# Performance work log

Hardware: AMD Instinct MI355X
Metric: run time of the kernel (lower is better)

Reference implementation:

```python
import jax, jax.numpy as jnp
import numpy as np

B_, C_, T_, F_ = 1, 64, 256, 128
D_CONV, D_STATE, DT_RANK = 4, 16, 4
D_INNER = 2 * C_
EPS = 1e-5


def setup_inputs():
    key = jax.random.key(0)
    ks = jax.random.split(key, 12)
    s = 0.05
    return {
        'x': jax.random.normal(ks[0], (B_, C_, T_, F_), jnp.float32),
        'norm_w': jnp.ones((4, C_), jnp.float32),
        'in_proj_w': jax.random.normal(ks[1], (4, 2 * D_INNER, C_), jnp.float32) * s,
        'conv_w': jax.random.normal(ks[2], (4, D_INNER, 1, D_CONV), jnp.float32) * 0.3,
        'conv_b': jnp.zeros((4, D_INNER), jnp.float32),
        'x_proj_w': jax.random.normal(ks[3], (4, DT_RANK + 2 * D_STATE, D_INNER), jnp.float32) * s,
        'dt_proj_w': jax.random.normal(ks[4], (4, D_INNER, DT_RANK), jnp.float32) * 0.1,
        'dt_proj_b': jnp.log(jnp.expm1(jax.random.uniform(ks[5], (4, D_INNER), jnp.float32, 1e-3, 0.1))),
        'A_log': jnp.log(jax.random.uniform(ks[6], (4, D_INNER, D_STATE), jnp.float32, 0.5, 16.0)),
        'Dp': jnp.ones((4, D_INNER), jnp.float32),
        'out_proj_w': jax.random.normal(ks[7], (4, C_, D_INNER), jnp.float32) * s,
        'tlin_w': jax.random.normal(ks[8], (2 * C_, C_), jnp.float32) * s,
        'tlin_b': jnp.zeros((C_,), jnp.float32),
        'flin_w': jax.random.normal(ks[9], (2 * C_, C_), jnp.float32) * s,
        'flin_b': jnp.zeros((C_,), jnp.float32),
    }


def _rmsnorm(x, w):
    return x * jax.lax.rsqrt(jnp.mean(x * x, axis=-1, keepdims=True) + EPS) * w


def _mamba(u, p):
    # u: (N, L, d_model) ; selective-scan Mamba mixer
    N, L, _ = u.shape
    xz = jnp.einsum('nld,ed->nle', u, p['in_proj_w'])  # (N,L,2*di)
    x, z = jnp.split(xz, 2, axis=-1)
    # causal depthwise conv over time
    xT = jnp.swapaxes(x, 1, 2)  # (N, di, L)
    xc = jax.lax.conv_general_dilated(xT, p['conv_w'], (1,), [(D_CONV - 1, 0)],
                                      feature_group_count=D_INNER)
    x = jnp.swapaxes(jax.nn.silu(xc + p['conv_b'][None, :, None]), 1, 2)  # (N,L,di)
    xdbl = jnp.einsum('nld,ed->nle', x, p['x_proj_w'])
    dt, Bm, Cm = jnp.split(xdbl, [DT_RANK, DT_RANK + D_STATE], axis=-1)
    dt = jax.nn.softplus(jnp.einsum('nlr,dr->nld', dt, p['dt_proj_w']) + p['dt_proj_b'])
    A = -jnp.exp(p['A_log'])  # (di, ds)

    def step(h, inp):
        dt_t, B_t, C_t, x_t = inp  # (N,di),(N,ds),(N,ds),(N,di)
        dA = jnp.exp(dt_t[:, :, None] * A)  # (N,di,ds)
        h = dA * h + dt_t[:, :, None] * B_t[:, None, :] * x_t[:, :, None]
        return h, jnp.einsum('nds,ns->nd', h, C_t)

    h0 = jnp.zeros((N, D_INNER, D_STATE), u.dtype)
    _, ys = jax.lax.scan(step, h0, (jnp.swapaxes(dt, 0, 1), jnp.swapaxes(Bm, 0, 1),
                                    jnp.swapaxes(Cm, 0, 1), jnp.swapaxes(x, 0, 1)))
    y = jnp.swapaxes(ys, 0, 1) + x * p['Dp']
    y = y * jax.nn.silu(z)
    return jnp.einsum('nld,od->nlo', y, p['out_proj_w'])


def _block(u, p):
    # mamba Block with residual: out = mixer(rmsnorm(u)) + u
    return _mamba(_rmsnorm(u, p['norm_w']), p) + u


def _bimamba(u, pf, pb):
    yf = _block(u, pf)
    yb = jnp.flip(_block(jnp.flip(u, 1), pb), 1)
    return jnp.concatenate([yf, yb], axis=-1)


def _pick(i, norm_w, in_proj_w, conv_w, conv_b, x_proj_w, dt_proj_w, dt_proj_b, A_log, Dp, out_proj_w):
    return dict(norm_w=norm_w[i], in_proj_w=in_proj_w[i], conv_w=conv_w[i], conv_b=conv_b[i],
                x_proj_w=x_proj_w[i], dt_proj_w=dt_proj_w[i], dt_proj_b=dt_proj_b[i],
                A_log=A_log[i], Dp=Dp[i], out_proj_w=out_proj_w[i])


def _tfmamba(x, norm_w, in_proj_w, conv_w, conv_b, x_proj_w, dt_proj_w, dt_proj_b,
             A_log, Dp, out_proj_w, tlin_w, tlin_b, flin_w, flin_b):
    b, c, t, f = x.shape
    P = [_pick(i, norm_w, in_proj_w, conv_w, conv_b, x_proj_w, dt_proj_w, dt_proj_b, A_log, Dp, out_proj_w)
         for i in range(4)]
    # time axis
    xt = jnp.reshape(jnp.transpose(x, (0, 3, 2, 1)), (b * f, t, c))
    xt_out = _bimamba(xt, P[0], P[1])  # (b*f, t, 2c)
    xt = xt + jnp.einsum('nti,io->nto', xt_out, tlin_w) + tlin_b
    # frequency axis
    xf = jnp.reshape(jnp.transpose(jnp.reshape(xt, (b, f, t, c)), (0, 2, 1, 3)), (b * t, f, c))
    xf_out = _bimamba(xf, P[2], P[3])  # (b*t, f, 2c)
    xf = xf + jnp.einsum('nfi,io->nfo', xf_out, flin_w) + flin_b
    return jnp.transpose(jnp.reshape(xf, (b, t, f, c)), (0, 3, 1, 2))


def reference(x, norm_w, in_proj_w, conv_w, conv_b, x_proj_w, dt_proj_w, dt_proj_b,
              A_log, Dp, out_proj_w, tlin_w, tlin_b, flin_w, flin_b):
    return _tfmamba(x, norm_w, in_proj_w, conv_w, conv_b, x_proj_w, dt_proj_w, dt_proj_b,
                    A_log, Dp, out_proj_w, tlin_w, tlin_b, flin_w, flin_b)
```

## Files before the change

kernel.cpp:

```cpp
#include <hip/hip_runtime.h>
#include <math.h>

#define C_DIM 64
#define T_DIM 256
#define F_DIM 128
#define DI    128
#define DS    16
#define CK    16

typedef __attribute__((ext_vector_type(8))) short bf16x8;
typedef __attribute__((ext_vector_type(4))) float f32x4;

__device__ __forceinline__ float silu_f(float v){ return v / (1.0f + __expf(-v)); }

__device__ __forceinline__ unsigned short f2bf(float f){
  union{float f; unsigned u;} v; v.f = f;
  unsigned r = v.u + 0x7FFFu + ((v.u >> 16) & 1u);
  return (unsigned short)(r >> 16);
}

__global__ __launch_bounds__(256) void k_prep(const float* __restrict__ ipw,
                                              const float* __restrict__ opw,
                                              unsigned short* __restrict__ wbuf){
  const int i = blockIdx.x*256 + threadIdx.x;
  if(i < 65536)       wbuf[i] = f2bf(ipw[i]);
  else if(i < 98304)  wbuf[i] = f2bf(opw[i - 65536]);
}

__global__ __launch_bounds__(256) void k_transpose_in(const float* __restrict__ x,
                                                      float* __restrict__ xt){
  __shared__ float tile[64][133];
  const int t = blockIdx.x;
  {
    const int fi = threadIdx.x & 127, cg = threadIdx.x >> 7;
    for(int c = cg*32; c < cg*32 + 32; ++c)
      tile[c][fi] = x[(size_t)c*32768 + (size_t)t*128 + fi];
  }
  __syncthreads();
  {
    const int ci = threadIdx.x & 63, fg = threadIdx.x >> 6;
    for(int f = fg*32; f < fg*32 + 32; ++f)
      xt[(size_t)f*16384 + (size_t)t*64 + ci] = tile[ci][f];
  }
}

__global__ __launch_bounds__(256, 2) void k_mamba(
    const float* __restrict__ src, int N, int L, long long sn, long long sl,
    int pbase,
    const float* __restrict__ norm_w,   const unsigned short* __restrict__ wbf,
    const float* __restrict__ conv_w,   const float* __restrict__ conv_b,
    const float* __restrict__ x_proj_w, const float* __restrict__ dt_proj_w,
    const float* __restrict__ dt_proj_b,const float* __restrict__ A_log,
    const float* __restrict__ Dp,       float* __restrict__ obuf)
{
  __shared__ __align__(16) unsigned short u_bf[CK][64];
  __shared__ float x_s[CK+3][132];
  __shared__ float z_s[CK][132];
  __shared__ float xc_s[CK][132];
  __shared__ float dt_s[CK][132];
  __shared__ float dtr_s[CK][4];
  __shared__ float B_s[CK][20];
  __shared__ float C_s[CK][20];
  __shared__ __align__(16) unsigned short y_bf[CK][128];
  __shared__ float y_out[CK][68];
  __shared__ float w_xp[36*132];
  __shared__ float w_cv[512];
  __shared__ float b_cv[128];
  __shared__ float w_dt[512];
  __shared__ float b_dt[128];
  __shared__ float dvec[128];
  __shared__ float nw[64];

  const int tid = threadIdx.x;
  const int bid = blockIdx.x;
  const int dir = (bid >= N) ? 1 : 0;
  const int n   = dir ? (bid - N) : bid;
  const int p   = pbase + dir;

  const int lane = tid & 63;
  const int wv   = tid >> 6;
  const int fr   = lane & 15;
  const int fk   = (lane >> 4) << 3;

  for(int i = tid; i < 36*128; i += 256){
    int o = i >> 7, k = i & 127;
    w_xp[o*132 + k] = x_proj_w[p*4608 + i];
  }
  for(int i = tid; i < 512; i += 256){ w_cv[i] = conv_w[p*512 + i]; w_dt[i] = dt_proj_w[p*512 + i]; }
  if(tid < 128){ b_cv[tid] = conv_b[p*128 + tid]; b_dt[tid] = dt_proj_b[p*128 + tid]; dvec[tid] = Dp[p*128 + tid]; }
  if(tid < 64) nw[tid] = norm_w[p*64 + tid];
  for(int i = tid; i < 3*128; i += 256){ x_s[i >> 7][i & 127] = 0.0f; }

  const unsigned short* WinB  = wbf + (size_t)p*16384;
  const unsigned short* WoutB = wbf + 65536 + (size_t)p*8192;
  bf16x8 aW[4][2];
  #pragma unroll
  for(int ot = 0; ot < 4; ++ot)
    #pragma unroll
    for(int kh = 0; kh < 2; ++kh)
      aW[ot][kh] = *(const bf16x8*)(WinB + (wv*64 + ot*16 + fr)*64 + kh*32 + fk);
  bf16x8 aO[4];
  #pragma unroll
  for(int kc = 0; kc < 4; ++kc)
    aO[kc] = *(const bf16x8*)(WoutB + (wv*16 + fr)*128 + kc*32 + fk);

  const int d_own = tid >> 1;
  const int sh    = (tid & 1) * 8;
  float A_r[8], h[8];
  #pragma unroll
  for(int i = 0; i < 8; ++i){
    A_r[i] = -__expf(A_log[p*2048 + d_own*16 + sh + i]) * 1.44269504f;
    h[i] = 0.0f;
  }
  __syncthreads();

  for(int c0 = 0; c0 < L; c0 += CK){
    if(c0 > 0){
      for(int i = tid; i < 3*128; i += 256){
        int r = i >> 7, ch = i & 127;
        x_s[r][ch] = x_s[CK + r][ch];
      }
    }
    {
      const int g = tid >> 4, j = tid & 15, c4 = j*4;
      const int l = c0 + g;
      const int lo = dir ? (L - 1 - l) : l;
      const float4 v = *(const float4*)(src + (size_t)n*sn + (size_t)lo*sl + c4);
      float ssq = v.x*v.x + v.y*v.y + v.z*v.z + v.w*v.w;
      ssq += __shfl_xor(ssq, 1); ssq += __shfl_xor(ssq, 2);
      ssq += __shfl_xor(ssq, 4); ssq += __shfl_xor(ssq, 8);
      const float sc = rsqrtf(ssq * (1.0f/64.0f) + 1e-5f);
      ushort4 pk;
      pk.x = f2bf(v.x * sc * nw[c4+0]);
      pk.y = f2bf(v.y * sc * nw[c4+1]);
      pk.z = f2bf(v.z * sc * nw[c4+2]);
      pk.w = f2bf(v.w * sc * nw[c4+3]);
      *(ushort4*)&u_bf[g][c4] = pk;
    }
    __syncthreads();

    {
      const bf16x8 b0 = *(const bf16x8*)&u_bf[fr][fk];
      const bf16x8 b1 = *(const bf16x8*)&u_bf[fr][32 + fk];
      #pragma unroll
      for(int ot = 0; ot < 4; ++ot){
        f32x4 acc = {0.f, 0.f, 0.f, 0.f};
        acc = __builtin_amdgcn_mfma_f32_16x16x32_bf16(aW[ot][0], b0, acc, 0, 0, 0);
        acc = __builtin_amdgcn_mfma_f32_16x16x32_bf16(aW[ot][1], b1, acc, 0, 0, 0);
        const int ob = wv*64 + ot*16 + ((lane >> 4) << 2);
        if(wv < 2){
          #pragma unroll
          for(int r = 0; r < 4; ++r) x_s[3 + fr][ob + r] = acc[r];
        } else {
          #pragma unroll
          for(int r = 0; r < 4; ++r) z_s[fr][ob + r - 128] = acc[r];
        }
      }
    }
    __syncthreads();

    {
      const int g = tid >> 4, j = tid & 15;
      #pragma unroll
      for(int i = 0; i < 8; ++i){
        const int ch = j + 16*i;
        float a = b_cv[ch];
        a += w_cv[ch*4+0] * x_s[g+0][ch];
        a += w_cv[ch*4+1] * x_s[g+1][ch];
        a += w_cv[ch*4+2] * x_s[g+2][ch];
        a += w_cv[ch*4+3] * x_s[g+3][ch];
        xc_s[g][ch] = silu_f(a);
      }
    }
    __syncthreads();

    {
      const int g = tid >> 4, j = tid & 15;
      #pragma unroll
      for(int rep = 0; rep < 3; ++rep){
        const int o36 = j + rep*16;
        if(o36 < 36){
          const float4* wr = (const float4*)&w_xp[o36*132];
          const float4* xr = (const float4*)&xc_s[g][0];
          float a = 0.0f;
          #pragma unroll
          for(int k4 = 0; k4 < 32; ++k4){
            const float4 w = wr[k4], xv = xr[k4];
            a += w.x*xv.x + w.y*xv.y + w.z*xv.z + w.w*xv.w;
          }
          if(o36 < 4)       dtr_s[g][o36] = a;
          else if(o36 < 20) B_s[g][o36 - 4] = a;
          else              C_s[g][o36 - 20] = a;
        }
      }
    }
    __syncthreads();

    {
      const int g = tid >> 4, j = tid & 15;
      const float r0 = dtr_s[g][0], r1 = dtr_s[g][1], r2 = dtr_s[g][2], r3 = dtr_s[g][3];
      #pragma unroll
      for(int i = 0; i < 8; ++i){
        const int d = j + 16*i;
        float a = b_dt[d] + w_dt[d*4+0]*r0 + w_dt[d*4+1]*r1 + w_dt[d*4+2]*r2 + w_dt[d*4+3]*r3;
        dt_s[g][d] = fmaxf(a, 0.0f) + log1pf(__expf(-fabsf(a)));
      }
    }
    __syncthreads();

    for(int l = 0; l < CK; ++l){
      const float dtv = dt_s[l][d_own];
      const float xv  = xc_s[l][d_own];
      const float4 b0 = *(const float4*)&B_s[l][sh];
      const float4 b1 = *(const float4*)&B_s[l][sh + 4];
      const float4 g0 = *(const float4*)&C_s[l][sh];
      const float4 g1 = *(const float4*)&C_s[l][sh + 4];
      const float bb[8] = {b0.x,b0.y,b0.z,b0.w,b1.x,b1.y,b1.z,b1.w};
      const float cc[8] = {g0.x,g0.y,g0.z,g0.w,g1.x,g1.y,g1.z,g1.w};
      const float dx = dtv * xv;
      float yp = 0.0f;
      #pragma unroll
      for(int i = 0; i < 8; ++i){
        h[i] = exp2f(dtv * A_r[i]) * h[i] + dx * bb[i];
        yp += h[i] * cc[i];
      }
      const float yo = yp + __shfl_xor(yp, 1);
      if((tid & 1) == 0) xc_s[l][d_own] = yo + xv * dvec[d_own];
    }
    __syncthreads();

    {
      const int g = tid >> 4, j = tid & 15;
      #pragma unroll
      for(int i = 0; i < 8; ++i){
        const int ch = j + 16*i;
        y_bf[g][ch] = f2bf(xc_s[g][ch] * silu_f(z_s[g][ch]));
      }
    }
    __syncthreads();

    {
      f32x4 acc = {0.f, 0.f, 0.f, 0.f};
      #pragma unroll
      for(int kc = 0; kc < 4; ++kc){
        const bf16x8 b = *(const bf16x8*)&y_bf[fr][kc*32 + fk];
        acc = __builtin_amdgcn_mfma_f32_16x16x32_bf16(aO[kc], b, acc, 0, 0, 0);
      }
      const int o2 = wv*16 + ((lane >> 4) << 2);
      #pragma unroll
      for(int r = 0; r < 4; ++r) y_out[fr][o2 + r] = acc[r];
    }
    __syncthreads();

    {
      const int o = tid & 63, lg = tid >> 6;
      #pragma unroll
      for(int li = 0; li < 4; ++li){
        const int l = c0 + lg*4 + li;
        const int lo = dir ? (L - 1 - l) : l;
        obuf[((size_t)dir*32768 + (size_t)n*L + lo)*64 + o] = y_out[lg*4 + li][o];
      }
    }
  }
}

__global__ __launch_bounds__(256) void k_comb_time(
    const float* __restrict__ xt, const float* __restrict__ obuf,
    const float* __restrict__ tlin_w, const float* __restrict__ tlin_b,
    float* __restrict__ xt2)
{
  __shared__ float xs[4][68], fs[4][68], bs[4][68];
  const int tg = threadIdx.x >> 6, o = threadIdx.x & 63;
  const int tk = blockIdx.x*4 + tg;
  xs[tg][o] = xt[(size_t)tk*64 + o];
  fs[tg][o] = obuf[(size_t)tk*64 + o];
  bs[tg][o] = obuf[(size_t)(32768 + tk)*64 + o];
  __syncthreads();
  float acc = xs[tg][o] + tlin_b[o];
  #pragma unroll 4
  for(int i = 0; i < 64; ++i){
    const float xv = xs[tg][i];
    acc += (fs[tg][i] + xv) * tlin_w[i*64 + o]
         + (bs[tg][i] + xv) * tlin_w[(64 + i)*64 + o];
  }
  xt2[(size_t)tk*64 + o] = acc;
}

__global__ __launch_bounds__(256) void k_final(
    const float* __restrict__ xt2, const float* __restrict__ obuf,
    const float* __restrict__ flin_w, const float* __restrict__ flin_b,
    float* __restrict__ out)
{
  __shared__ float res_s[128][68];
  const int t = blockIdx.x, tid = threadIdx.x;
  const int f = tid >> 1, half = tid & 1, cbase = half*32;

  const float4* xr = (const float4*)(xt2  + (size_t)f*16384 + (size_t)t*64);
  const float4* fr = (const float4*)(obuf + ((size_t)t*128 + f)*64);
  const float4* br = (const float4*)(obuf + ((size_t)32768 + (size_t)t*128 + f)*64);

  float res[32];
  {
    const float4* fb = (const float4*)(flin_b + cbase);
    #pragma unroll
    for(int q = 0; q < 8; ++q){
      const float4 xv = xr[(cbase >> 2) + q], b = fb[q];
      res[q*4+0] = xv.x + b.x; res[q*4+1] = xv.y + b.y;
      res[q*4+2] = xv.z + b.z; res[q*4+3] = xv.w + b.w;
    }
  }
  for(int i4 = 0; i4 < 16; ++i4){
    const float4 xv4 = xr[i4], of4 = fr[i4], ob4 = br[i4];
    const float af[4] = {of4.x + xv4.x, of4.y + xv4.y, of4.z + xv4.z, of4.w + xv4.w};
    const float ab[4] = {ob4.x + xv4.x, ob4.y + xv4.y, ob4.z + xv4.z, ob4.w + xv4.w};
    #pragma unroll
    for(int ii = 0; ii < 4; ++ii){
      const int i = i4*4 + ii;
      const float4* F0 = (const float4*)(flin_w + i*64 + cbase);
      const float4* F1 = (const float4*)(flin_w + (64 + i)*64 + cbase);
      #pragma unroll
      for(int q = 0; q < 8; ++q){
        const float4 w0 = F0[q], w1 = F1[q];
        res[q*4+0] += af[ii]*w0.x + ab[ii]*w1.x;
        res[q*4+1] += af[ii]*w0.y + ab[ii]*w1.y;
        res[q*4+2] += af[ii]*w0.z + ab[ii]*w1.z;
        res[q*4+3] += af[ii]*w0.w + ab[ii]*w1.w;
      }
    }
  }
  #pragma unroll
  for(int c = 0; c < 32; ++c) res_s[f][cbase + c] = res[c];
  __syncthreads();
  {
    const int fi = tid & 127, cq = tid >> 7;
    for(int c = cq*32; c < cq*32 + 32; ++c)
      out[(size_t)c*32768 + (size_t)t*128 + fi] = res_s[fi][c];
  }
}

extern "C" void kernel_launch(void* const* d_in, const int* in_sizes, int n_in,
                              void* d_out, int out_size, void* d_ws, size_t ws_size,
                              hipStream_t stream){
  (void)in_sizes; (void)n_in; (void)out_size; (void)ws_size;
  const float* x         = (const float*)d_in[0];
  const float* norm_w    = (const float*)d_in[1];
  const float* in_proj_w = (const float*)d_in[2];
  const float* conv_w    = (const float*)d_in[3];
  const float* conv_b    = (const float*)d_in[4];
  const float* x_proj_w  = (const float*)d_in[5];
  const float* dt_proj_w = (const float*)d_in[6];
  const float* dt_proj_b = (const float*)d_in[7];
  const float* A_log     = (const float*)d_in[8];
  const float* Dp        = (const float*)d_in[9];
  const float* out_proj_w= (const float*)d_in[10];
  const float* tlin_w    = (const float*)d_in[11];
  const float* tlin_b    = (const float*)d_in[12];
  const float* flin_w    = (const float*)d_in[13];
  const float* flin_b    = (const float*)d_in[14];
  float* out = (float*)d_out;

  float* xt_buf = (float*)d_ws;
  float* obuf   = xt_buf + (size_t)(1u << 21);
  float* xt2    = obuf   + (size_t)(1u << 22);

  unsigned short* wbf = (unsigned short*)d_out;

  hipLaunchKernelGGL(k_prep, dim3(384), dim3(256), 0, stream,
      in_proj_w, out_proj_w, wbf);

  hipLaunchKernelGGL(k_transpose_in, dim3(256), dim3(256), 0, stream, x, xt_buf);

  hipLaunchKernelGGL(k_mamba, dim3(256), dim3(256), 0, stream,
      xt_buf, 128, 256, (long long)16384, (long long)64, 0,
      norm_w, wbf, conv_w, conv_b, x_proj_w, dt_proj_w, dt_proj_b,
      A_log, Dp, obuf);

  hipLaunchKernelGGL(k_comb_time, dim3(8192), dim3(256), 0, stream,
      xt_buf, obuf, tlin_w, tlin_b, xt2);

  hipLaunchKernelGGL(k_mamba, dim3(512), dim3(256), 0, stream,
      xt2, 256, 128, (long long)64, (long long)16384, 2,
      norm_w, wbf, conv_w, conv_b, x_proj_w, dt_proj_w, dt_proj_b,
      A_log, Dp, obuf);

  hipLaunchKernelGGL(k_final, dim3(256), dim3(256), 0, stream,
      xt2, obuf, flin_w, flin_b, out);
}
```

Before: 500.8 us.

## Use bf16 MFMA for x_proj in mamba and for time-axis combine linear

Converts x_proj_w (padded to 48 rows) and transposed tlin_w to bf16 in the prep kernel. In k_mamba the fp32 scalar x_proj dot products are replaced by an MFMA on three waves, which also removes the large fp32 weight tile from LDS. k_comb_time is rewritten to handle 64 tokens per block with MFMA instead of one token per 64 threads reading fp32 weights from global memory. This lowers FLOP cost and LDS use, at the price of bf16 rounding on these projections.

```diff
diff --git a/kernel.cpp b/kernel.cpp
--- a/kernel.cpp
+++ b/kernel.cpp
@@ -21,10 +21,23 @@
 
 __global__ __launch_bounds__(256) void k_prep(const float* __restrict__ ipw,
                                               const float* __restrict__ opw,
+                                              const float* __restrict__ xpw,
+                                              const float* __restrict__ tlw,
                                               unsigned short* __restrict__ wbuf){
   const int i = blockIdx.x*256 + threadIdx.x;
-  if(i < 65536)       wbuf[i] = f2bf(ipw[i]);
-  else if(i < 98304)  wbuf[i] = f2bf(opw[i - 65536]);
+  if(i < 65536){
+    wbuf[i] = f2bf(ipw[i]);
+  } else if(i < 98304){
+    wbuf[i] = f2bf(opw[i - 65536]);
+  } else if(i < 122880){
+    const int j = i - 98304;
+    const int p = j / 6144, rr = (j - p*6144) >> 7, k = j & 127;
+    wbuf[i] = (rr < 36) ? f2bf(xpw[p*4608 + rr*128 + k]) : (unsigned short)0;
+  } else {
+    const int j = i - 122880;
+    const int o = j >> 7, k = j & 127;
+    wbuf[i] = f2bf(tlw[k*64 + o]);
+  }
 }
 
 __global__ __launch_bounds__(256) void k_transpose_in(const float* __restrict__ x,
@@ -49,7 +62,7 @@
     int pbase,
     const float* __restrict__ norm_w,   const unsigned short* __restrict__ wbf,
     const float* __restrict__ conv_w,   const float* __restrict__ conv_b,
-    const float* __restrict__ x_proj_w, const float* __restrict__ dt_proj_w,
+    const float* __restrict__ dt_proj_w,
     const float* __restrict__ dt_proj_b,const float* __restrict__ A_log,
     const float* __restrict__ Dp,       float* __restrict__ obuf)
 {
@@ -57,13 +70,13 @@
   __shared__ float x_s[CK+3][132];
   __shared__ float z_s[CK][132];
   __shared__ float xc_s[CK][132];
+  __shared__ __align__(16) unsigned short xc_bf[CK][128];
   __shared__ float dt_s[CK][132];
   __shared__ float dtr_s[CK][4];
   __shared__ float B_s[CK][20];
   __shared__ float C_s[CK][20];
   __shared__ __align__(16) unsigned short y_bf[CK][128];
   __shared__ float y_out[CK][68];
-  __shared__ float w_xp[36*132];
   __shared__ float w_cv[512];
   __shared__ float b_cv[128];
   __shared__ float w_dt[512];
@@ -82,10 +95,6 @@
   const int fr   = lane & 15;
   const int fk   = (lane >> 4) << 3;
 
-  for(int i = tid; i < 36*128; i += 256){
-    int o = i >> 7, k = i & 127;
-    w_xp[o*132 + k] = x_proj_w[p*4608 + i];
-  }
   for(int i = tid; i < 512; i += 256){ w_cv[i] = conv_w[p*512 + i]; w_dt[i] = dt_proj_w[p*512 + i]; }
   if(tid < 128){ b_cv[tid] = conv_b[p*128 + tid]; b_dt[tid] = dt_proj_b[p*128 + tid]; dvec[tid] = Dp[p*128 + tid]; }
   if(tid < 64) nw[tid] = norm_w[p*64 + tid];
@@ -93,6 +102,7 @@
 
   const unsigned short* WinB  = wbf + (size_t)p*16384;
   const unsigned short* WoutB = wbf + 65536 + (size_t)p*8192;
+  const unsigned short* XpB   = wbf + 98304 + (size_t)p*6144;
   bf16x8 aW[4][2];
   #pragma unroll
   for(int ot = 0; ot < 4; ++ot)
@@ -103,6 +113,12 @@
   #pragma unroll
   for(int kc = 0; kc < 4; ++kc)
     aO[kc] = *(const bf16x8*)(WoutB + (wv*16 + fr)*128 + kc*32 + fk);
+  bf16x8 aXP[4];
+  if(wv < 3){
+    #pragma unroll
+    for(int kc = 0; kc < 4; ++kc)
+      aXP[kc] = *(const bf16x8*)(XpB + (wv*16 + fr)*128 + kc*32 + fk);
+  }
 
   const int d_own = tid >> 1;
   const int sh    = (tid & 1) * 8;
@@ -169,29 +185,28 @@
         a += w_cv[ch*4+1] * x_s[g+1][ch];
         a += w_cv[ch*4+2] * x_s[g+2][ch];
         a += w_cv[ch*4+3] * x_s[g+3][ch];
-        xc_s[g][ch] = silu_f(a);
-      }
-    }
-    __syncthreads();
-
-    {
-      const int g = tid >> 4, j = tid & 15;
-      #pragma unroll
-      for(int rep = 0; rep < 3; ++rep){
-        const int o36 = j + rep*16;
-        if(o36 < 36){
-          const float4* wr = (const float4*)&w_xp[o36*132];
-          const float4* xr = (const float4*)&xc_s[g][0];
-          float a = 0.0f;
-          #pragma unroll
-          for(int k4 = 0; k4 < 32; ++k4){
-            const float4 w = wr[k4], xv = xr[k4];
-            a += w.x*xv.x + w.y*xv.y + w.z*xv.z + w.w*xv.w;
-          }
-          if(o36 < 4)       dtr_s[g][o36] = a;
-          else if(o36 < 20) B_s[g][o36 - 4] = a;
-          else              C_s[g][o36 - 20] = a;
-        }
+        const float s = silu_f(a);
+        xc_s[g][ch]  = s;
+        xc_bf[g][ch] = f2bf(s);
+      }
+    }
+    __syncthreads();
+
+    if(wv < 3){
+      f32x4 acc = {0.f, 0.f, 0.f, 0.f};
+      #pragma unroll
+      for(int kc = 0; kc < 4; ++kc){
+        const bf16x8 b = *(const bf16x8*)&xc_bf[fr][kc*32 + fk];
+        acc = __builtin_amdgcn_mfma_f32_16x16x32_bf16(aXP[kc], b, acc, 0, 0, 0);
+      }
+      const int ob36 = wv*16 + ((lane >> 4) << 2);
+      #pragma unroll
+      for(int r = 0; r < 4; ++r){
+        const int o36 = ob36 + r;
+        const float v = acc[r];
+        if(o36 < 4)       dtr_s[fr][o36] = v;
+        else if(o36 < 20) B_s[fr][o36 - 4] = v;
+        else if(o36 < 36) C_s[fr][o36 - 20] = v;
       }
     }
     __syncthreads();
@@ -266,24 +281,70 @@
 
 __global__ __launch_bounds__(256) void k_comb_time(
     const float* __restrict__ xt, const float* __restrict__ obuf,
-    const float* __restrict__ tlin_w, const float* __restrict__ tlin_b,
+    const unsigned short* __restrict__ wbf, const float* __restrict__ tlin_b,
     float* __restrict__ xt2)
 {
-  __shared__ float xs[4][68], fs[4][68], bs[4][68];
-  const int tg = threadIdx.x >> 6, o = threadIdx.x & 63;
-  const int tk = blockIdx.x*4 + tg;
-  xs[tg][o] = xt[(size_t)tk*64 + o];
-  fs[tg][o] = obuf[(size_t)tk*64 + o];
-  bs[tg][o] = obuf[(size_t)(32768 + tk)*64 + o];
+  __shared__ __align__(16) unsigned short in_bf[64][128];
+  __shared__ float xs[64][72];
+  const int tid = threadIdx.x;
+  const int lane = tid & 63, wv = tid >> 6;
+  const int fr = lane & 15, fk = (lane >> 4) << 3;
+  const int tk0 = blockIdx.x*64;
+
+  const unsigned short* TL = wbf + 122880;
+  bf16x8 aT[4];
+  #pragma unroll
+  for(int kc = 0; kc < 4; ++kc)
+    aT[kc] = *(const bf16x8*)(TL + (wv*16 + fr)*128 + kc*32 + fk);
+
+  {
+    const int tg = tid >> 2, q = tid & 3;
+    #pragma unroll
+    for(int s = 0; s < 4; ++s){
+      const int c4 = q*16 + s*4;
+      const float4 xv = *(const float4*)(xt   + ((size_t)tk0 + tg)*64 + c4);
+      const float4 fv = *(const float4*)(obuf + ((size_t)tk0 + tg)*64 + c4);
+      const float4 bv = *(const float4*)(obuf + ((size_t)32768 + tk0 + tg)*64 + c4);
+      ushort4 pf, pb;
+      pf.x = f2bf(fv.x + xv.x); pf.y = f2bf(fv.y + xv.y);
+      pf.z = f2bf(fv.z + xv.z); pf.w = f2bf(fv.w + xv.w);
+      pb.x = f2bf(bv.x + xv.x); pb.y = f2bf(bv.y + xv.y);
+      pb.z = f2bf(bv.z + xv.z); pb.w = f2bf(bv.w + xv.w);
+      *(ushort4*)&in_bf[tg][c4]      = pf;
+      *(ushort4*)&in_bf[tg][64 + c4] = pb;
+      *(float4*)&xs[tg][c4] = xv;
+    }
+  }
   __syncthreads();
-  float acc = xs[tg][o] + tlin_b[o];
-  #pragma unroll 4
-  for(int i = 0; i < 64; ++i){
-    const float xv = xs[tg][i];
-    acc += (fs[tg][i] + xv) * tlin_w[i*64 + o]
-         + (bs[tg][i] + xv) * tlin_w[(64 + i)*64 + o];
-  }
-  xt2[(size_t)tk*64 + o] = acc;
+
+  {
+    const int ob = wv*16 + ((lane >> 4) << 2);
+    const float4 tb = *(const float4*)(tlin_b + ob);
+    const float tbr[4] = {tb.x, tb.y, tb.z, tb.w};
+    #pragma unroll
+    for(int tt = 0; tt < 4; ++tt){
+      f32x4 acc = {0.f, 0.f, 0.f, 0.f};
+      #pragma unroll
+      for(int kc = 0; kc < 4; ++kc){
+        const bf16x8 b = *(const bf16x8*)&in_bf[tt*16 + fr][kc*32 + fk];
+        acc = __builtin_amdgcn_mfma_f32_16x16x32_bf16(aT[kc], b, acc, 0, 0, 0);
+      }
+      const int token = tt*16 + fr;
+      #pragma unroll
+      for(int r = 0; r < 4; ++r)
+        xs[token][ob + r] += tbr[r] + acc[r];
+    }
+  }
+  __syncthreads();
+
+  {
+    const int tg = tid >> 2, q = tid & 3;
+    #pragma unroll
+    for(int s = 0; s < 4; ++s){
+      const int c4 = q*16 + s*4;
+      *(float4*)(xt2 + ((size_t)tk0 + tg)*64 + c4) = *(const float4*)&xs[tg][c4];
+    }
+  }
 }
 
 __global__ __launch_bounds__(256) void k_final(
@@ -365,22 +426,22 @@
 
   unsigned short* wbf = (unsigned short*)d_out;
 
-  hipLaunchKernelGGL(k_prep, dim3(384), dim3(256), 0, stream,
-      in_proj_w, out_proj_w, wbf);
+  hipLaunchKernelGGL(k_prep, dim3(512), dim3(256), 0, stream,
+      in_proj_w, out_proj_w, x_proj_w, tlin_w, wbf);
 
   hipLaunchKernelGGL(k_transpose_in, dim3(256), dim3(256), 0, stream, x, xt_buf);
 
   hipLaunchKernelGGL(k_mamba, dim3(256), dim3(256), 0, stream,
       xt_buf, 128, 256, (long long)16384, (long long)64, 0,
-      norm_w, wbf, conv_w, conv_b, x_proj_w, dt_proj_w, dt_proj_b,
+      norm_w, wbf, conv_w, conv_b, dt_proj_w, dt_proj_b,
       A_log, Dp, obuf);
 
-  hipLaunchKernelGGL(k_comb_time, dim3(8192), dim3(256), 0, stream,
-      xt_buf, obuf, tlin_w, tlin_b, xt2);
+  hipLaunchKernelGGL(k_comb_time, dim3(512), dim3(256), 0, stream,
+      xt_buf, obuf, wbf, tlin_b, xt2);
 
   hipLaunchKernelGGL(k_mamba, dim3(512), dim3(256), 0, stream,
       xt2, 256, 128, (long long)64, (long long)16384, 2,
-      norm_w, wbf, conv_w, conv_b, x_proj_w, dt_proj_w, dt_proj_b,
+      norm_w, wbf, conv_w, conv_b, dt_proj_w, dt_proj_b,
       A_log, Dp, obuf);
 
   hipLaunchKernelGGL(k_final, dim3(256), dim3(256), 0, stream,
```

New measurement: 431.3 us. 1.16x faster.
